# Kernel tuning notes

Measured on AMD Instinct MI355X. Metric: run time of the kernel, lower is better.

Reference implementation:

```python
import jax, jax.numpy as jnp
import numpy as np

DIM = 1024
CTX_DIM = 1024
HEADS = 16
DIM_HEAD = 64
INNER = HEADS * DIM_HEAD
SCALE = DIM_HEAD ** -0.5


def _layer_norm(x, g, b, eps=1e-5):
    mu = x.mean(-1, keepdims=True)
    var = ((x - mu) ** 2).mean(-1, keepdims=True)
    return (x - mu) * jax.lax.rsqrt(var + eps) * g + b


def setup_inputs() -> dict:
    key = jax.random.key(0)
    ks = jax.random.split(key, 10)
    b, i, j = 2, 1024, 1024
    s = lambda fan_in: 1.0 / np.sqrt(fan_in)
    return {
        "x": jax.random.normal(ks[0], (b, i, DIM), jnp.float32),
        "context": jax.random.normal(ks[1], (b, j, CTX_DIM), jnp.float32),
        "mask": jnp.ones((b, i), dtype=bool),
        "context_mask": jnp.ones((b, j), dtype=bool),
        "ln_g": jnp.ones((DIM,), jnp.float32),
        "ln_b": jnp.zeros((DIM,), jnp.float32),
        "cln_g": jnp.ones((CTX_DIM,), jnp.float32),
        "cln_b": jnp.zeros((CTX_DIM,), jnp.float32),
        "W_qk": jax.random.normal(ks[2], (DIM, INNER), jnp.float32) * s(DIM),
        "W_cqk": jax.random.normal(ks[3], (CTX_DIM, INNER), jnp.float32) * s(CTX_DIM),
        "W_v": jax.random.normal(ks[4], (DIM, INNER), jnp.float32) * s(DIM),
        "W_cv": jax.random.normal(ks[5], (CTX_DIM, INNER), jnp.float32) * s(CTX_DIM),
        "W_out": jax.random.normal(ks[6], (INNER, DIM), jnp.float32) * s(INNER),
        "b_out": jnp.zeros((DIM,), jnp.float32),
        "W_cout": jax.random.normal(ks[7], (INNER, CTX_DIM), jnp.float32) * s(INNER),
        "b_cout": jnp.zeros((CTX_DIM,), jnp.float32),
        "W_th": jax.random.normal(ks[8], (HEADS, HEADS), jnp.float32) * s(HEADS),   # talking heads [out_h, in_h]
        "W_cth": jax.random.normal(ks[9], (HEADS, HEADS), jnp.float32) * s(HEADS),
    }


def reference(x, context, mask, context_mask, ln_g, ln_b, cln_g, cln_b,
              W_qk, W_cqk, W_v, W_cv, W_out, b_out, W_cout, b_cout, W_th, W_cth):
    b, i, _ = x.shape
    j = context.shape[1]
    xn = _layer_norm(x, ln_g, ln_b)
    cn = _layer_norm(context, cln_g, cln_b)

    split = lambda t: t.reshape(t.shape[0], t.shape[1], HEADS, DIM_HEAD).transpose(0, 2, 1, 3)  # b h n d
    qk = split(xn @ W_qk)
    cqk = split(cn @ W_cqk)
    v = split(xn @ W_v)
    cv = split(cn @ W_cv)

    sim = jnp.einsum('bhid,bhjd->bhij', qk, cqk) * SCALE

    attn_mask = mask[:, None, :, None] & context_mask[:, None, None, :]  # b 1 i j
    sim = jnp.where(attn_mask, sim, -jnp.finfo(sim.dtype).max)

    attn = jax.nn.softmax(sim, axis=-1)       # rows: x attends to context
    cattn = jax.nn.softmax(sim, axis=-2)      # cols: context attends to x

    # talking heads: 1x1 conv over head dim, weight [out_h, in_h]
    attn = jnp.einsum('bhij,gh->bgij', attn, W_th)
    cattn = jnp.einsum('bhij,gh->bgij', cattn, W_cth)

    out = jnp.einsum('bhij,bhjd->bhid', attn, cv)
    cout = jnp.einsum('bhji,bhjd->bhid', cattn, v)

    merge = lambda t: t.transpose(0, 2, 1, 3).reshape(t.shape[0], t.shape[2], INNER)
    out = merge(out) @ W_out + b_out
    cout = merge(cout) @ W_cout + b_cout
    return out, cout
```

## Files before the change

kernel.cpp:

```cpp
#include <hip/hip_runtime.h>
#include <hip/hip_bf16.h>

#define BB 2
#define SEQ 1024
#define DIMD 1024
#define NH 16
#define DH 64
#define INNERD 1024
#define SCALEF 0.125f

typedef __hip_bfloat16 bf16;
typedef __attribute__((ext_vector_type(8))) short short8;
typedef __attribute__((ext_vector_type(4))) float f32x4;

__device__ __forceinline__ float b2f(bf16 x) { return __bfloat162float(x); }
__device__ __forceinline__ bf16 f2b(float x) { return __float2bfloat16(x); }
__device__ __forceinline__ float s2f(unsigned short s) {
    return __uint_as_float(((unsigned int)s) << 16);
}
__device__ __forceinline__ unsigned short f2bs(float v) {
    bf16 t = __float2bfloat16(v);
    return *(unsigned short*)&t;
}

__device__ __forceinline__ void stf(float* p, size_t i, float v) { p[i] = v; }
__device__ __forceinline__ void stf(bf16* p, size_t i, float v) { p[i] = f2b(v); }

__device__ __forceinline__ void async16(const short* g, short* l) {
    __builtin_amdgcn_global_load_lds(
        (const __attribute__((address_space(1))) unsigned int*)(g),
        (__attribute__((address_space(3))) unsigned int*)(l), 16, 0, 0);
}

__global__ __launch_bounds__(256) void prep_kernel(
    const float* __restrict__ s0, const float* __restrict__ s1,
    const float* __restrict__ s2, const float* __restrict__ s3,
    const float* __restrict__ s4, const float* __restrict__ s5,
    bf16* __restrict__ d0, bf16* __restrict__ d1, bf16* __restrict__ d2,
    bf16* __restrict__ d3, bf16* __restrict__ d4, bf16* __restrict__ d5,
    const float* __restrict__ x0, const float* __restrict__ g0,
    const float* __restrict__ b0, bf16* __restrict__ o0,
    const float* __restrict__ x1, const float* __restrict__ g1,
    const float* __restrict__ b1, bf16* __restrict__ o1) {
    int z = blockIdx.z;
    int tid = threadIdx.x;
    if (z < 6) {
        const float* W = z == 0 ? s0 : z == 1 ? s1 : z == 2 ? s2 : z == 3 ? s3
                         : z == 4 ? s4 : s5;
        bf16* Wt = z == 0 ? d0 : z == 1 ? d1 : z == 2 ? d2 : z == 3 ? d3
                   : z == 4 ? d4 : d5;
        __shared__ float T[32][33];
        int n0 = blockIdx.x * 32, k0 = blockIdx.y * 32;
        int tx = tid & 31, ty = tid >> 5;
#pragma unroll
        for (int s = 0; s < 4; ++s)
            T[ty + s * 8][tx] = W[(size_t)(k0 + ty + s * 8) * 1024 + n0 + tx];
        __syncthreads();
#pragma unroll
        for (int s = 0; s < 4; ++s)
            Wt[(size_t)(n0 + ty + s * 8) * 1024 + k0 + tx] = f2b(T[tx][ty + s * 8]);
    } else {
        int rowg = (z - 6) * 1024 + blockIdx.y * 32 + blockIdx.x;
        int sel = rowg >= BB * SEQ;
        int row = sel ? rowg - BB * SEQ : rowg;
        const float* xr = (sel ? x1 : x0) + (size_t)row * DIMD;
        const float* g = sel ? g1 : g0;
        const float* b = sel ? b1 : b0;
        bf16* orow = (sel ? o1 : o0) + (size_t)row * DIMD;
        float v[4];
        float s = 0.f, s2 = 0.f;
#pragma unroll
        for (int k = 0; k < 4; ++k) {
            v[k] = xr[tid + k * 256];
            s += v[k];
            s2 += v[k] * v[k];
        }
        __shared__ float sh1[256], sh2[256];
        sh1[tid] = s; sh2[tid] = s2;
        __syncthreads();
        for (int off = 128; off > 0; off >>= 1) {
            if (tid < off) { sh1[tid] += sh1[tid + off]; sh2[tid] += sh2[tid + off]; }
            __syncthreads();
        }
        float mu = sh1[0] * (1.f / DIMD);
        float var = sh2[0] * (1.f / DIMD) - mu * mu;
        float rstd = rsqrtf(var + 1e-5f);
#pragma unroll
        for (int k = 0; k < 4; ++k) {
            int c = tid + k * 256;
            orow[c] = f2b((v[k] - mu) * rstd * g[c] + b[c]);
        }
    }
}

template <typename TC, bool HASBIAS, int BM, int BN, int MT, int NT, int ZS, bool TRANSC>
__global__ __launch_bounds__(256) void mfma_gemm(
    const bf16* __restrict__ A, long sA1, long sA2, int lda,
    const bf16* __restrict__ Bt, long sB1, long sB2, int ldb,
    TC* __restrict__ C, long sC1, long sC2, int ldc,
    bf16* __restrict__ TD, long sT1,
    const float* __restrict__ bias0, const float* __restrict__ bias1,
    float alpha, int K) {
    constexpr int WX = BN / (NT * 16);
    static_assert((4 / WX) * MT * 16 == BM, "BM/waves mismatch");
    static_assert(BM % 64 == 0 && BN % 64 == 0, "chunk uniformity");
    int z = blockIdx.z;
    int zb = z / ZS, zh = z % ZS;
    const short* Ag = (const short*)(A + zb * sA1 + zh * sA2);
    const short* Bg = (const short*)(Bt + zb * sB1 + zh * sB2);
    TC* Cp = C + zb * sC1 + zh * sC2;
    const float* bias = (zh == 0) ? bias0 : bias1;

    const int m0 = blockIdx.y * BM;
    const int n0 = blockIdx.x * BN;
    int tid = threadIdx.x;
    int wave = tid >> 6, lane = tid & 63;
    int wm = (wave / WX) * (MT * 16), wn = (wave % WX) * (NT * 16);
    int lrow = lane & 15, lquad = lane >> 4;

    __shared__ short S[2][(BM + BN) * 32];

    f32x4 acc[MT][NT] = {};

    for (int k0 = 0; k0 < K; k0 += 64) {
        constexpr int CH = (BM + BN) / 64;
#pragma unroll
        for (int half = 0; half < 2; ++half) {
            int kh = k0 + half * 32;
#pragma unroll
            for (int ch = 0; ch < CH; ++ch) {
                int e = ch * 256 + tid;
                int r = e >> 2, c = (e & 3) * 8;
                const short* g = (r < BM)
                                     ? Ag + (size_t)(m0 + r) * lda + kh + c
                                     : Bg + (size_t)(n0 + r - BM) * ldb + kh + c;
                async16(g, S[half] + (size_t)e * 8);
            }
        }
        __syncthreads();
#pragma unroll
        for (int half = 0; half < 2; ++half) {
            short8 af[MT], bfv[NT];
#pragma unroll
            for (int mt = 0; mt < MT; ++mt)
                af[mt] = *(const short8*)(S[half] + (wm + mt * 16 + lrow) * 32 +
                                          lquad * 8);
#pragma unroll
            for (int nt = 0; nt < NT; ++nt)
                bfv[nt] = *(const short8*)(S[half] + (BM + wn + nt * 16 + lrow) * 32 +
                                           lquad * 8);
#pragma unroll
            for (int mt = 0; mt < MT; ++mt)
#pragma unroll
                for (int nt = 0; nt < NT; ++nt)
                    acc[mt][nt] = __builtin_amdgcn_mfma_f32_16x16x32_bf16(
                        af[mt], bfv[nt], acc[mt][nt], 0, 0, 0);
        }
        __syncthreads();
    }
    if (TRANSC && zh == 1) {
        bf16* td = TD + zb * sT1;
        int bsel = m0 >> 10;
        int tokb = (m0 & 1023) + wm + lquad * 4;
#pragma unroll
        for (int mt = 0; mt < MT; ++mt) {
#pragma unroll
            for (int nt = 0; nt < NT; ++nt) {
                int col = n0 + wn + nt * 16 + lrow;
                ushort4 o;
                o.x = f2bs(acc[mt][nt][0]);
                o.y = f2bs(acc[mt][nt][1]);
                o.z = f2bs(acc[mt][nt][2]);
                o.w = f2bs(acc[mt][nt][3]);
                *(ushort4*)((unsigned short*)td +
                            ((size_t)(bsel * NH + (col >> 6)) * DH + (col & 63)) * SEQ +
                            tokb + mt * 16) = o;
            }
        }
        return;
    }
#pragma unroll
    for (int mt = 0; mt < MT; ++mt) {
#pragma unroll
        for (int nt = 0; nt < NT; ++nt) {
            int col = n0 + wn + nt * 16 + lrow;
#pragma unroll
            for (int r = 0; r < 4; ++r) {
                int row = m0 + wm + mt * 16 + lquad * 4 + r;
                float v = acc[mt][nt][r] * alpha;
                if (HASBIAS) v += bias[col];
                stf(Cp, (size_t)row * ldc + col, v);
            }
        }
    }
}

__global__ __launch_bounds__(256) void qkt_stats_kernel(
    const bf16* __restrict__ qk, const bf16* __restrict__ cqk,
    bf16* __restrict__ sim16, float* __restrict__ rowPart,
    float* __restrict__ colPart, long sQ, long sS, long sP) {
    int z = blockIdx.z;
    int b = z >> 4, h = z & 15;
    const short* Ag = (const short*)(qk + b * sQ + h * DH);
    const short* Bg = (const short*)(cqk + b * sQ + h * DH);
    bf16* Cp = sim16 + b * sS + (size_t)h * SEQ * SEQ;
    rowPart += b * sP;
    colPart += b * sP;

    const int m0 = blockIdx.y * 128;
    const int n0 = blockIdx.x * 128;
    int tid = threadIdx.x;
    int wave = tid >> 6, lane = tid & 63;
    int wy = wave >> 1, wx = wave & 1;
    int wm = wy * 64, wn = wx * 64;
    int lrow = lane & 15, lquad = lane >> 4;

    __shared__ short S[2][256 * 32];
    __shared__ float rowLDS[128][2];
    __shared__ float colLDS[128][2];

    f32x4 acc[4][4] = {};

#pragma unroll
    for (int half = 0; half < 2; ++half) {
        int kh = half * 32;
#pragma unroll
        for (int ch = 0; ch < 4; ++ch) {
            int e = ch * 256 + tid;
            int r = e >> 2, c = (e & 3) * 8;
            const short* g = (r < 128)
                                 ? Ag + (size_t)(m0 + r) * INNERD + kh + c
                                 : Bg + (size_t)(n0 + r - 128) * INNERD + kh + c;
            async16(g, S[half] + (size_t)e * 8);
        }
    }
    __syncthreads();
#pragma unroll
    for (int half = 0; half < 2; ++half) {
        short8 af[4], bfv[4];
#pragma unroll
        for (int mt = 0; mt < 4; ++mt)
            af[mt] = *(const short8*)(S[half] + (wm + mt * 16 + lrow) * 32 + lquad * 8);
#pragma unroll
        for (int nt = 0; nt < 4; ++nt)
            bfv[nt] = *(const short8*)(S[half] + (128 + wn + nt * 16 + lrow) * 32 +
                                       lquad * 8);
#pragma unroll
        for (int mt = 0; mt < 4; ++mt)
#pragma unroll
            for (int nt = 0; nt < 4; ++nt)
                acc[mt][nt] = __builtin_amdgcn_mfma_f32_16x16x32_bf16(
                    af[mt], bfv[nt], acc[mt][nt], 0, 0, 0);
    }
    float rband[16];
    float cacc[4] = {};
#pragma unroll
    for (int k = 0; k < 16; ++k) rband[k] = 0.f;
#pragma unroll
    for (int mt = 0; mt < 4; ++mt) {
#pragma unroll
        for (int nt = 0; nt < 4; ++nt) {
            int col = n0 + wn + nt * 16 + lrow;
#pragma unroll
            for (int r = 0; r < 4; ++r) {
                int row = m0 + wm + mt * 16 + lquad * 4 + r;
                unsigned short us = f2bs(acc[mt][nt][r] * SCALEF);
                *((unsigned short*)Cp + (size_t)row * SEQ + col) = us;
                float e = __expf(s2f(us));
                rband[mt * 4 + r] += e;
                cacc[nt] += e;
            }
        }
    }
#pragma unroll
    for (int m = 1; m < 16; m <<= 1)
#pragma unroll
        for (int k = 0; k < 16; ++k) rband[k] += __shfl_xor(rband[k], m, 64);
    if (lrow == 0) {
#pragma unroll
        for (int mt = 0; mt < 4; ++mt)
#pragma unroll
            for (int r = 0; r < 4; ++r)
                rowLDS[wm + mt * 16 + lquad * 4 + r][wx] = rband[mt * 4 + r];
    }
#pragma unroll
    for (int m = 16; m < 64; m <<= 1)
#pragma unroll
        for (int nt = 0; nt < 4; ++nt) cacc[nt] += __shfl_xor(cacc[nt], m, 64);
    if (lquad == 0) {
#pragma unroll
        for (int nt = 0; nt < 4; ++nt)
            colLDS[wn + nt * 16 + lrow][wy] = cacc[nt];
    }
    __syncthreads();
    if (tid < 128)
        rowPart[((size_t)h * 8 + blockIdx.x) * SEQ + m0 + tid] =
            rowLDS[tid][0] + rowLDS[tid][1];
    else
        colPart[((size_t)h * 8 + blockIdx.y) * SEQ + n0 + tid - 128] =
            colLDS[tid - 128][0] + colLDS[tid - 128][1];
}

__global__ __launch_bounds__(256) void finish_inv2_kernel(const float* __restrict__ partA,
                                                          float* __restrict__ invA,
                                                          const float* __restrict__ partB,
                                                          float* __restrict__ invB) {
    int idx = blockIdx.x * 256 + threadIdx.x;
    int h = idx >> 10, t = idx & 1023;
    float sA = 0.f, sB = 0.f;
#pragma unroll
    for (int p = 0; p < 8; ++p) {
        sA += partA[((size_t)h * 8 + p) * SEQ + t];
        sB += partB[((size_t)h * 8 + p) * SEQ + t];
    }
    invA[idx] = 1.f / sA;
    invB[idx] = 1.f / sB;
}

__global__ __launch_bounds__(256) void mix_kernel(bf16* simattn,
                                                  bf16* __restrict__ catT,
                                                  const float* __restrict__ rli,
                                                  const float* __restrict__ cli,
                                                  const float* __restrict__ Wth,
                                                  const float* __restrict__ Wcth,
                                                  long sS, long sI) {
    int zb = blockIdx.z;
    simattn += zb * sS;
    catT += zb * sS;
    rli += zb * sI;
    cli += zb * sI;
    int d = blockIdx.y * gridDim.x + blockIdx.x;
    int grp = d >> 4, s = d & 15;
    int pairIdx = grp * 8 + (s & 7);
    int half = s >> 3;
    int j0 = (2 * (pairIdx & 31) + half) * 16;
    int i0 = (pairIdx >> 5) * 16;
    int tid = threadIdx.x;
    int jl = tid & 15, il = tid >> 4;
    int i = i0 + il, j = j0 + jl;
    float sa[16] = {}, sc[16] = {};
#pragma unroll
    for (int h = 0; h < 16; ++h) {
        float s2 = b2f(simattn[((size_t)h * SEQ + i) * SEQ + j]);
        float e = __expf(s2);
        float p = e * rli[h * SEQ + i];
        float q = e * cli[h * SEQ + j];
#pragma unroll
        for (int g = 0; g < 16; ++g) {
            sa[g] += p * Wth[g * 16 + h];
            sc[g] += q * Wcth[g * 16 + h];
        }
    }
#pragma unroll
    for (int g = 0; g < 16; ++g)
        simattn[((size_t)g * SEQ + i) * SEQ + j] = f2b(sa[g]);
    __shared__ float T[16][16][17];
#pragma unroll
    for (int g = 0; g < 16; ++g) T[g][il][jl] = sc[g];
    __syncthreads();
#pragma unroll
    for (int g = 0; g < 16; ++g)
        catT[((size_t)g * SEQ + j0 + il) * SEQ + i0 + jl] = f2b(T[g][jl][il]);
}

extern "C" void kernel_launch(void* const* d_in, const int* in_sizes, int n_in,
                              void* d_out, int out_size, void* d_ws, size_t ws_size,
                              hipStream_t stream) {
    const float* x = (const float*)d_in[0];
    const float* ctx = (const float*)d_in[1];
    const float* ln_g = (const float*)d_in[4];
    const float* ln_b = (const float*)d_in[5];
    const float* cln_g = (const float*)d_in[6];
    const float* cln_b = (const float*)d_in[7];
    const float* W_qk = (const float*)d_in[8];
    const float* W_cqk = (const float*)d_in[9];
    const float* W_v = (const float*)d_in[10];
    const float* W_cv = (const float*)d_in[11];
    const float* W_out = (const float*)d_in[12];
    const float* b_out = (const float*)d_in[13];
    const float* W_cout = (const float*)d_in[14];
    const float* b_cout = (const float*)d_in[15];
    const float* W_th = (const float*)d_in[16];
    const float* W_cth = (const float*)d_in[17];
    float* out = (float*)d_out;

    char* ws = (char*)d_ws;
    size_t off = 0;
    auto alloc = [&](size_t bytes) {
        void* p = ws + off;
        off += (bytes + 255) & ~(size_t)255;
        return p;
    };
    const size_t NTOK = (size_t)BB * SEQ * DIMD;
    const size_t WSZ = (size_t)DIMD * INNERD;
    const size_t U = (size_t)NH * SEQ * SEQ;
    const long HB = (long)NH * DH * SEQ;

    bf16* xn = (bf16*)alloc(NTOK * 2);
    bf16* cn = (bf16*)alloc(NTOK * 2);
    bf16* qk = (bf16*)alloc(NTOK * 2);
    bf16* cqk = (bf16*)alloc(NTOK * 2);
    bf16* wqk_t = (bf16*)alloc(WSZ * 2);
    bf16* wv_t = (bf16*)alloc(WSZ * 2);
    bf16* wcqk_t = (bf16*)alloc(WSZ * 2);
    bf16* wcv_t = (bf16*)alloc(WSZ * 2);
    bf16* wout_t = (bf16*)alloc(WSZ * 2);
    bf16* wcout_t = (bf16*)alloc(WSZ * 2);
    bf16* cvT = (bf16*)alloc(NTOK * 2);
    bf16* vT = (bf16*)alloc(NTOK * 2);
    bf16* outm = xn;

    const size_t partB = (size_t)NH * 8 * SEQ * 4;
    const size_t invB = (size_t)NH * SEQ * 4;
    const size_t bigNeed = 4 * U * 2 + 2 * (2 * partB) + 2 * (2 * invB);
    bool big = (ws_size > off) && (ws_size - off >= bigNeed);

    prep_kernel<<<dim3(32, 32, 10), 256, 0, stream>>>(
        W_qk, W_v, W_cqk, W_cv, W_out, W_cout,
        wqk_t, wv_t, wcqk_t, wcv_t, wout_t, wcout_t,
        x, ln_g, ln_b, xn, ctx, cln_g, cln_b, cn);
    mfma_gemm<bf16, false, 128, 64, 2, 4, 2, true><<<dim3(16, 16, 4), 256, 0, stream>>>(
        xn, (long)NTOK, 0, DIMD,
        wqk_t, (long)(2 * WSZ), (long)WSZ, DIMD,
        qk, (long)NTOK, 0, INNERD,
        vT, -(long)NTOK,
        nullptr, nullptr, 1.0f, DIMD);

    if (big) {
        bf16* sim0 = (bf16*)alloc(U * 2);
        bf16* sim1 = (bf16*)alloc(U * 2);
        bf16* cb0 = (bf16*)alloc(U * 2);
        bf16* cb1 = (bf16*)alloc(U * 2);
        float* rowPart = (float*)alloc(2 * partB);
        float* colPart = (float*)alloc(2 * partB);
        float* rowInv = (float*)alloc(2 * invB);
        float* colInv = (float*)alloc(2 * invB);
        (void)sim1; (void)cb1;

        qkt_stats_kernel<<<dim3(8, 8, 32), 256, 0, stream>>>(
            qk, cqk, sim0, rowPart, colPart,
            (long)SEQ * INNERD, (long)U, (long)NH * 8 * SEQ);
        finish_inv2_kernel<<<2 * NH * SEQ / 256, 256, 0, stream>>>(rowPart, rowInv,
                                                                   colPart, colInv);
        mix_kernel<<<dim3(SEQ / 16, SEQ / 16, 2), 256, 0, stream>>>(
            sim0, cb0, rowInv, colInv, W_th, W_cth, (long)U, (long)NH * SEQ);
        mfma_gemm<bf16, false, 64, 64, 1, 4, 16, false><<<dim3(1, 16, 4 * NH), 256, 0,
                                                          stream>>>(
            sim0, (long)U, (long)SEQ * SEQ, SEQ,
            cvT, HB, (long)DH * SEQ, SEQ,
            outm, (long)SEQ * INNERD, (long)DH, INNERD,
            nullptr, 0, nullptr, nullptr, 1.0f, SEQ);
    } else {
        bf16* simA = (bf16*)alloc(U * 2);
        bf16* cbuf = (bf16*)alloc(U * 2);
        float* rowPart = (float*)alloc(partB);
        float* colPart = (float*)alloc(partB);
        float* rowInv = (float*)alloc(invB);
        float* colInv = (float*)alloc(invB);
        for (int b = 0; b < BB; ++b) {
            qkt_stats_kernel<<<dim3(8, 8, 16), 256, 0, stream>>>(
                qk + (size_t)b * SEQ * INNERD, cqk + (size_t)b * SEQ * INNERD,
                simA, rowPart, colPart, 0, 0, 0);
            finish_inv2_kernel<<<NH * SEQ / 256, 256, 0, stream>>>(rowPart, rowInv,
                                                                   colPart, colInv);
            mix_kernel<<<dim3(SEQ / 16, SEQ / 16, 1), 256, 0, stream>>>(
                simA, cbuf, rowInv, colInv, W_th, W_cth, 0, 0);
            mfma_gemm<bf16, false, 64, 64, 1, 4, 16, false><<<dim3(1, 16, 2 * NH), 256,
                                                              0, stream>>>(
                simA, (long)U, (long)SEQ * SEQ, SEQ,
                cvT + (size_t)b * HB, (long)NTOK, (long)DH * SEQ, SEQ,
                outm + (size_t)b * SEQ * INNERD, (long)NTOK, (long)DH, INNERD,
                nullptr, 0, nullptr, nullptr, 1.0f, SEQ);
        }
    }

    mfma_gemm<float, true, 128, 64, 2, 4, 2, false><<<dim3(16, 16, 2), 256, 0, stream>>>(
        outm, 0, (long)NTOK, INNERD, wout_t, 0, (long)WSZ, INNERD,
        out, 0, (long)NTOK, DIMD, nullptr, 0, b_out, b_cout, 1.0f, INNERD);
}
```

Before: 279.1 us.

## Compute talking-heads head mixing with MFMA bf16 instead of scalar FMAs

The per-element 16x16 head-mixing loop in the softmax/talking-heads kernel is replaced by two 16x16x32 bf16 MFMA instructions per row, with half the K dimension zero-padded. Each wave handles four i-rows, and lanes in the upper half of the wave feed zeros. The transposed cattn output is now staged through shared memory and written as 16-byte vector stores. The exp/normalize products and the weights are rounded to bf16 before mixing, which adds precision loss, and half of each MFMA's K lanes do no useful work.

```diff
diff --git a/kernel.cpp b/kernel.cpp
--- a/kernel.cpp
+++ b/kernel.cpp
@@ -336,31 +336,63 @@
     int j0 = (2 * (pairIdx & 31) + half) * 16;
     int i0 = (pairIdx >> 5) * 16;
     int tid = threadIdx.x;
-    int jl = tid & 15, il = tid >> 4;
-    int i = i0 + il, j = j0 + jl;
-    float sa[16] = {}, sc[16] = {};
-#pragma unroll
-    for (int h = 0; h < 16; ++h) {
-        float s2 = b2f(simattn[((size_t)h * SEQ + i) * SEQ + j]);
-        float e = __expf(s2);
-        float p = e * rli[h * SEQ + i];
-        float q = e * cli[h * SEQ + j];
-#pragma unroll
-        for (int g = 0; g < 16; ++g) {
-            sa[g] += p * Wth[g * 16 + h];
-            sc[g] += q * Wcth[g * 16 + h];
-        }
-    }
-#pragma unroll
-    for (int g = 0; g < 16; ++g)
-        simattn[((size_t)g * SEQ + i) * SEQ + j] = f2b(sa[g]);
-    __shared__ float T[16][16][17];
-#pragma unroll
-    for (int g = 0; g < 16; ++g) T[g][il][jl] = sc[g];
+    int wave = tid >> 6, lane = tid & 63;
+    int q = lane >> 4, low = lane & 15;
+    int j = j0 + low;
+
+    short8 aTH = {}, aCTH = {};
+    float clv[8];
+    if (q < 2) {
+#pragma unroll
+        for (int idx = 0; idx < 8; ++idx) {
+            int h = q * 8 + idx;
+            aTH[idx] = (short)f2bs(Wth[low * 16 + h]);
+            aCTH[idx] = (short)f2bs(Wcth[low * 16 + h]);
+            clv[idx] = cli[h * SEQ + j];
+        }
+    }
+
+    __shared__ float Tc[16][16][17];
+
+    const unsigned short* sp = (const unsigned short*)simattn;
+    unsigned short* ap = (unsigned short*)simattn;
+
+#pragma unroll
+    for (int rr = 0; rr < 4; ++rr) {
+        int il = wave * 4 + rr;
+        int i = i0 + il;
+        short8 bp = {}, bq = {};
+        if (q < 2) {
+            const unsigned short* sr =
+                sp + (size_t)(q * 8) * SEQ * SEQ + (size_t)i * SEQ + j;
+            const float* rp = rli + (size_t)(q * 8) * SEQ + i;
+#pragma unroll
+            for (int idx = 0; idx < 8; ++idx) {
+                float e = __expf(s2f(sr[(size_t)idx * SEQ * SEQ]));
+                bp[idx] = (short)f2bs(e * rp[(size_t)idx * SEQ]);
+                bq[idx] = (short)f2bs(e * clv[idx]);
+            }
+        }
+        f32x4 z = {};
+        f32x4 accA = __builtin_amdgcn_mfma_f32_16x16x32_bf16(aTH, bp, z, 0, 0, 0);
+        f32x4 accC = __builtin_amdgcn_mfma_f32_16x16x32_bf16(aCTH, bq, z, 0, 0, 0);
+#pragma unroll
+        for (int r = 0; r < 4; ++r) {
+            ap[((size_t)(q * 4 + r) * SEQ + i) * SEQ + j] = f2bs(accA[r]);
+            Tc[il][q * 4 + r][low] = accC[r];
+        }
+    }
     __syncthreads();
-#pragma unroll
-    for (int g = 0; g < 16; ++g)
-        catT[((size_t)g * SEQ + j0 + il) * SEQ + i0 + jl] = f2b(T[g][jl][il]);
+    int gp = tid >> 4, jp = tid & 15;
+    short8 o0, o1;
+#pragma unroll
+    for (int k = 0; k < 8; ++k) o0[k] = (short)f2bs(Tc[k][gp][jp]);
+#pragma unroll
+    for (int k = 0; k < 8; ++k) o1[k] = (short)f2bs(Tc[k + 8][gp][jp]);
+    unsigned short* dst =
+        (unsigned short*)catT + ((size_t)gp * SEQ + j0 + jp) * SEQ + i0;
+    *(short8*)dst = o0;
+    *(short8*)(dst + 8) = o1;
 }
 
 extern "C" void kernel_launch(void* const* d_in, const int* in_sizes, int n_in,
```

Measured after the change: 294.3 us. +5.5%, slower.

## Fuse softmax exp, talking-heads mix and PV GEMM into one split-K kernel

Applied to the files above, without the earlier changes.

Replaces the separate mix kernel (which wrote the mixed row-attention and a transposed column-attention matrix back to global memory) and the following PV GEMM with a single fused kernel. It recomputes exp and normalization from the stored logits, applies the head-mixing weights with MFMA into shared memory, and immediately multiplies by the value tiles. Each block covers a slice of K, so partial results are combined with fp32 atomics into a zeroed buffer, and a cast kernel then converts that buffer to bf16. This removes two full-size attention-matrix round trips to memory, at the cost of a memset, atomic contention and an extra cast pass; it also drops the small-workspace fallback path.

```diff
diff --git a/kernel.cpp b/kernel.cpp
--- a/kernel.cpp
+++ b/kernel.cpp
@@ -317,50 +317,151 @@
     invB[idx] = 1.f / sB;
 }
 
-__global__ __launch_bounds__(256) void mix_kernel(bf16* simattn,
-                                                  bf16* __restrict__ catT,
-                                                  const float* __restrict__ rli,
-                                                  const float* __restrict__ cli,
-                                                  const float* __restrict__ Wth,
-                                                  const float* __restrict__ Wcth,
-                                                  long sS, long sI) {
-    int zb = blockIdx.z;
-    simattn += zb * sS;
-    catT += zb * sS;
-    rli += zb * sI;
-    cli += zb * sI;
-    int d = blockIdx.y * gridDim.x + blockIdx.x;
-    int grp = d >> 4, s = d & 15;
-    int pairIdx = grp * 8 + (s & 7);
-    int half = s >> 3;
-    int j0 = (2 * (pairIdx & 31) + half) * 16;
-    int i0 = (pairIdx >> 5) * 16;
-    int tid = threadIdx.x;
-    int jl = tid & 15, il = tid >> 4;
-    int i = i0 + il, j = j0 + jl;
-    float sa[16] = {}, sc[16] = {};
-#pragma unroll
-    for (int h = 0; h < 16; ++h) {
-        float s2 = b2f(simattn[((size_t)h * SEQ + i) * SEQ + j]);
-        float e = __expf(s2);
-        float p = e * rli[h * SEQ + i];
-        float q = e * cli[h * SEQ + j];
-#pragma unroll
-        for (int g = 0; g < 16; ++g) {
-            sa[g] += p * Wth[g * 16 + h];
-            sc[g] += q * Wcth[g * 16 + h];
-        }
-    }
-#pragma unroll
-    for (int g = 0; g < 16; ++g)
-        simattn[((size_t)g * SEQ + i) * SEQ + j] = f2b(sa[g]);
-    __shared__ float T[16][16][17];
-#pragma unroll
-    for (int g = 0; g < 16; ++g) T[g][il][jl] = sc[g];
-    __syncthreads();
-#pragma unroll
-    for (int g = 0; g < 16; ++g)
-        catT[((size_t)g * SEQ + j0 + il) * SEQ + i0 + jl] = f2b(T[g][jl][il]);
+__global__ __launch_bounds__(256) void fused_pv(
+    const bf16* __restrict__ sim, const float* __restrict__ rowInv,
+    const float* __restrict__ colInv, const float* __restrict__ Wth,
+    const float* __restrict__ Wcth, const bf16* __restrict__ cvT,
+    float* __restrict__ outF) {
+    const int z = blockIdx.z;
+    const int path = z >> 1, b = z & 1;
+    const unsigned short* sp =
+        (const unsigned short*)sim + (size_t)b * NH * SEQ * SEQ;
+    const float* inv = (path ? colInv : rowInv) + (size_t)b * NH * SEQ;
+    const float* Wmix = path ? Wcth : Wth;
+    const short* Bg = (const short*)cvT + (size_t)z * NH * DH * SEQ;
+    outF += (size_t)z * SEQ * INNERD;
+
+    const int bx = blockIdx.x;
+    const int rt = (bx & 7) * 8 + (bx >> 3);
+    const int r0 = rt * 16;
+    const int kbase = blockIdx.y * 256;
+
+    const int tid = threadIdx.x;
+    const int wave = tid >> 6, lane = tid & 63;
+    const int q = lane >> 4, low = lane & 15;
+    const bool loQ = q < 2;
+    const int hq = (q & 1) * 8;
+
+    constexpr int HsA = 584, IsA = 36;
+    constexpr int HsC = 644, KsC = 20;
+    constexpr int Gs = 656, Rs = 40;
+    __shared__ unsigned short RAW[10304];
+    __shared__ unsigned short ATT[10496];
+
+    float s8[8];
+    {
+        const float* ip = inv + (size_t)hq * SEQ + r0 + low;
+#pragma unroll
+        for (int idx = 0; idx < 8; ++idx) s8[idx] = ip[(size_t)idx * SEQ];
+    }
+    short8 aW = {};
+    if (loQ) {
+#pragma unroll
+        for (int idx = 0; idx < 8; ++idx)
+            aW[idx] = (short)f2bs(Wmix[low * 16 + hq + idx]);
+    }
+
+    f32x4 acc[4][4] = {};
+    const int gw = wave * 4;
+
+    for (int st = 0; st < 8; ++st) {
+        const int k0 = kbase + st * 32;
+        if (path == 0) {
+#pragma unroll
+            for (int it = 0; it < 4; ++it) {
+                int rowId = it * 64 + (tid >> 2);
+                int h = rowId >> 4, r = rowId & 15, p = tid & 3;
+                const unsigned short* src =
+                    sp + ((size_t)h * SEQ + r0 + r) * SEQ + k0 + p * 8;
+                int4 w = *(const int4*)src;
+                unsigned short* d = RAW + h * HsA + r * IsA + p * 8;
+                *(int2*)d = make_int2(w.x, w.y);
+                *(int2*)(d + 4) = make_int2(w.z, w.w);
+            }
+        } else {
+#pragma unroll
+            for (int it = 0; it < 4; ++it) {
+                int task = it * 256 + tid;
+                int row = task >> 1, p = task & 1;
+                int h = row >> 5, kk = row & 31;
+                const unsigned short* src =
+                    sp + ((size_t)h * SEQ + k0 + kk) * SEQ + r0 + p * 8;
+                int4 w = *(const int4*)src;
+                unsigned short* d = RAW + h * HsC + kk * KsC + p * 8;
+                *(int2*)d = make_int2(w.x, w.y);
+                *(int2*)(d + 4) = make_int2(w.z, w.w);
+            }
+        }
+        __syncthreads();
+#pragma unroll
+        for (int u = 0; u < 4; ++u) {
+            int kq = wave * 8 + 2 * u + (q >> 1);
+            short8 P;
+#pragma unroll
+            for (int idx = 0; idx < 8; ++idx) {
+                unsigned short uu =
+                    (path == 0) ? RAW[(hq + idx) * HsA + low * IsA + kq]
+                                : RAW[(hq + idx) * HsC + kq * KsC + low];
+                float e = __expf(s2f(uu));
+                P[idx] = (short)f2bs(e * s8[idx]);
+            }
+            int4 Pi = *(int4*)&P;
+            int4 Sw;
+            Sw.x = __shfl_xor(Pi.x, 32);
+            Sw.y = __shfl_xor(Pi.y, 32);
+            Sw.z = __shfl_xor(Pi.z, 32);
+            Sw.w = __shfl_xor(Pi.w, 32);
+            short8 z8 = {};
+            short8 bpE = loQ ? P : z8;
+            short8 bpO = loQ ? *(short8*)&Sw : z8;
+            f32x4 zz = {};
+            f32x4 dE = __builtin_amdgcn_mfma_f32_16x16x32_bf16(aW, bpE, zz, 0, 0, 0);
+            f32x4 dO = __builtin_amdgcn_mfma_f32_16x16x32_bf16(aW, bpO, zz, 0, 0, 0);
+            int kE = wave * 8 + 2 * u;
+#pragma unroll
+            for (int rr = 0; rr < 4; ++rr) {
+                ATT[(q * 4 + rr) * Gs + low * Rs + kE] = f2bs(dE[rr]);
+                ATT[(q * 4 + rr) * Gs + low * Rs + kE + 1] = f2bs(dO[rr]);
+            }
+        }
+        __syncthreads();
+#pragma unroll
+        for (int gg = 0; gg < 4; ++gg) {
+            int g = gw + gg;
+            short8 af = *(const short8*)(ATT + g * Gs + low * Rs + q * 8);
+#pragma unroll
+            for (int dt = 0; dt < 4; ++dt) {
+                const short* bp =
+                    Bg + ((size_t)(g * 64 + dt * 16 + low)) * SEQ + k0 + q * 8;
+                short8 bf8 = *(const short8*)bp;
+                acc[gg][dt] = __builtin_amdgcn_mfma_f32_16x16x32_bf16(
+                    af, bf8, acc[gg][dt], 0, 0, 0);
+            }
+        }
+        __syncthreads();
+    }
+#pragma unroll
+    for (int gg = 0; gg < 4; ++gg)
+#pragma unroll
+        for (int dt = 0; dt < 4; ++dt)
+#pragma unroll
+            for (int rr = 0; rr < 4; ++rr)
+                unsafeAtomicAdd(outF + (size_t)(r0 + q * 4 + rr) * INNERD +
+                                    (gw + gg) * 64 + dt * 16 + low,
+                                acc[gg][dt][rr]);
+}
+
+__global__ __launch_bounds__(256) void cast_kernel(const float* __restrict__ src,
+                                                   bf16* __restrict__ dst) {
+    size_t i = ((size_t)blockIdx.x * 256 + threadIdx.x) * 8;
+    float4 a = *(const float4*)(src + i);
+    float4 c = *(const float4*)(src + i + 4);
+    short8 o;
+    o[0] = (short)f2bs(a.x); o[1] = (short)f2bs(a.y);
+    o[2] = (short)f2bs(a.z); o[3] = (short)f2bs(a.w);
+    o[4] = (short)f2bs(c.x); o[5] = (short)f2bs(c.y);
+    o[6] = (short)f2bs(c.z); o[7] = (short)f2bs(c.w);
+    *(short8*)((unsigned short*)dst + i) = o;
 }
 
 extern "C" void kernel_launch(void* const* d_in, const int* in_sizes, int n_in,
@@ -409,11 +510,21 @@
     bf16* cvT = (bf16*)alloc(NTOK * 2);
     bf16* vT = (bf16*)alloc(NTOK * 2);
     bf16* outm = xn;
+    (void)cn; (void)vT;
 
     const size_t partB = (size_t)NH * 8 * SEQ * 4;
     const size_t invB = (size_t)NH * SEQ * 4;
-    const size_t bigNeed = 4 * U * 2 + 2 * (2 * partB) + 2 * (2 * invB);
-    bool big = (ws_size > off) && (ws_size - off >= bigNeed);
+
+    bf16* sim0 = (bf16*)alloc(U * 2);
+    bf16* sim1 = (bf16*)alloc(U * 2);
+    (void)sim1;
+    float* rowPart = (float*)alloc(2 * partB);
+    float* colPart = (float*)alloc(2 * partB);
+    float* rowInv = (float*)alloc(2 * invB);
+    float* colInv = (float*)alloc(2 * invB);
+    float* outF = (float*)alloc((size_t)4 * SEQ * INNERD * 4);
+
+    hipMemsetAsync(outF, 0, (size_t)4 * SEQ * INNERD * 4, stream);
 
     prep_kernel<<<dim3(32, 32, 10), 256, 0, stream>>>(
         W_qk, W_v, W_cqk, W_cv, W_out, W_cout,
@@ -426,53 +537,16 @@
         vT, -(long)NTOK,
         nullptr, nullptr, 1.0f, DIMD);
 
-    if (big) {
-        bf16* sim0 = (bf16*)alloc(U * 2);
-        bf16* sim1 = (bf16*)alloc(U * 2);
-        bf16* cb0 = (bf16*)alloc(U * 2);
-        bf16* cb1 = (bf16*)alloc(U * 2);
-        float* rowPart = (float*)alloc(2 * partB);
-        float* colPart = (float*)alloc(2 * partB);
-        float* rowInv = (float*)alloc(2 * invB);
-        float* colInv = (float*)alloc(2 * invB);
-        (void)sim1; (void)cb1;
-
-        qkt_stats_kernel<<<dim3(8, 8, 32), 256, 0, stream>>>(
-            qk, cqk, sim0, rowPart, colPart,
-            (long)SEQ * INNERD, (long)U, (long)NH * 8 * SEQ);
-        finish_inv2_kernel<<<2 * NH * SEQ / 256, 256, 0, stream>>>(rowPart, rowInv,
-                                                                   colPart, colInv);
-        mix_kernel<<<dim3(SEQ / 16, SEQ / 16, 2), 256, 0, stream>>>(
-            sim0, cb0, rowInv, colInv, W_th, W_cth, (long)U, (long)NH * SEQ);
-        mfma_gemm<bf16, false, 64, 64, 1, 4, 16, false><<<dim3(1, 16, 4 * NH), 256, 0,
-                                                          stream>>>(
-            sim0, (long)U, (long)SEQ * SEQ, SEQ,
-            cvT, HB, (long)DH * SEQ, SEQ,
-            outm, (long)SEQ * INNERD, (long)DH, INNERD,
-            nullptr, 0, nullptr, nullptr, 1.0f, SEQ);
-    } else {
-        bf16* simA = (bf16*)alloc(U * 2);
-        bf16* cbuf = (bf16*)alloc(U * 2);
-        float* rowPart = (float*)alloc(partB);
-        float* colPart = (float*)alloc(partB);
-        float* rowInv = (float*)alloc(invB);
-        float* colInv = (float*)alloc(invB);
-        for (int b = 0; b < BB; ++b) {
-            qkt_stats_kernel<<<dim3(8, 8, 16), 256, 0, stream>>>(
-                qk + (size_t)b * SEQ * INNERD, cqk + (size_t)b * SEQ * INNERD,
-                simA, rowPart, colPart, 0, 0, 0);
-            finish_inv2_kernel<<<NH * SEQ / 256, 256, 0, stream>>>(rowPart, rowInv,
-                                                                   colPart, colInv);
-            mix_kernel<<<dim3(SEQ / 16, SEQ / 16, 1), 256, 0, stream>>>(
-                simA, cbuf, rowInv, colInv, W_th, W_cth, 0, 0);
-            mfma_gemm<bf16, false, 64, 64, 1, 4, 16, false><<<dim3(1, 16, 2 * NH), 256,
-                                                              0, stream>>>(
-                simA, (long)U, (long)SEQ * SEQ, SEQ,
-                cvT + (size_t)b * HB, (long)NTOK, (long)DH * SEQ, SEQ,
-                outm + (size_t)b * SEQ * INNERD, (long)NTOK, (long)DH, INNERD,
-                nullptr, 0, nullptr, nullptr, 1.0f, SEQ);
-        }
-    }
+    qkt_stats_kernel<<<dim3(8, 8, 32), 256, 0, stream>>>(
+        qk, cqk, sim0, rowPart, colPart,
+        (long)SEQ * INNERD, (long)U, (long)NH * 8 * SEQ);
+    finish_inv2_kernel<<<2 * NH * SEQ / 256, 256, 0, stream>>>(rowPart, rowInv,
+                                                               colPart, colInv);
+    fused_pv<<<dim3(64, 4, 4), 256, 0, stream>>>(
+        sim0, rowInv, colInv, W_th, W_cth, cvT, outF);
+
+    cast_kernel<<<(int)((size_t)4 * SEQ * INNERD / (256 * 8)), 256, 0, stream>>>(
+        outF, outm);
 
     mfma_gemm<float, true, 128, 64, 2, 4, 2, false><<<dim3(16, 16, 2), 256, 0, stream>>>(
         outm, 0, (long)NTOK, INNERD, wout_t, 0, (long)WSZ, INNERD,
```

New measurement: 321.5 us. 15.2% more time.

## Widen mix kernel tiles to 16x32 with packed bf16x2 loads and stores

Applied to the files above, without the earlier changes.

The talking-heads mix kernel now has each thread handle two adjacent columns, using 32-bit packed bf16 loads and stores. It stages the row and column softmax inverses in shared memory. The transposed cattn output is written through a two-pass shared-memory transpose with 16-byte vector stores. The intent is to cut memory transactions and global loads in this bandwidth-bound kernel, in exchange for doubled register accumulators and extra barriers.

```diff
diff --git a/kernel.cpp b/kernel.cpp
--- a/kernel.cpp
+++ b/kernel.cpp
@@ -333,34 +333,72 @@
     int grp = d >> 4, s = d & 15;
     int pairIdx = grp * 8 + (s & 7);
     int half = s >> 3;
-    int j0 = (2 * (pairIdx & 31) + half) * 16;
-    int i0 = (pairIdx >> 5) * 16;
+    int j0 = (pairIdx & 31) * 32;
+    int i0 = (((pairIdx >> 5) << 1) + half) * 16;
     int tid = threadIdx.x;
-    int jl = tid & 15, il = tid >> 4;
-    int i = i0 + il, j = j0 + jl;
-    float sa[16] = {}, sc[16] = {};
+    int il = tid >> 4, jp = tid & 15;
+
+    __shared__ float Tc[8][16][33];
+    __shared__ float rli_l[16][16];
+    __shared__ float cli_l[16][32];
+
+    rli_l[tid >> 4][tid & 15] = rli[(size_t)(tid >> 4) * SEQ + i0 + (tid & 15)];
+#pragma unroll
+    for (int k = 0; k < 2; ++k) {
+        int c = k * 256 + tid;
+        cli_l[c >> 5][c & 31] = cli[(size_t)(c >> 5) * SEQ + j0 + (c & 31)];
+    }
+    __syncthreads();
+
+    const unsigned int* lp = (const unsigned int*)simattn +
+                             (((size_t)(i0 + il) * SEQ + j0) >> 1) + jp;
+    float sa0[16] = {}, sa1[16] = {}, sc0[16] = {}, sc1[16] = {};
 #pragma unroll
     for (int h = 0; h < 16; ++h) {
-        float s2 = b2f(simattn[((size_t)h * SEQ + i) * SEQ + j]);
-        float e = __expf(s2);
-        float p = e * rli[h * SEQ + i];
-        float q = e * cli[h * SEQ + j];
+        unsigned int v = lp[(size_t)h * (SEQ * SEQ / 2)];
+        float e0 = __expf(s2f((unsigned short)(v & 0xffffu)));
+        float e1 = __expf(s2f((unsigned short)(v >> 16)));
+        float r = rli_l[h][il];
+        float p0 = e0 * r, p1 = e1 * r;
+        float q0 = e0 * cli_l[h][2 * jp], q1 = e1 * cli_l[h][2 * jp + 1];
 #pragma unroll
         for (int g = 0; g < 16; ++g) {
-            sa[g] += p * Wth[g * 16 + h];
-            sc[g] += q * Wcth[g * 16 + h];
-        }
-    }
+            float w = Wth[g * 16 + h];
+            float wc = Wcth[g * 16 + h];
+            sa0[g] += p0 * w;
+            sa1[g] += p1 * w;
+            sc0[g] += q0 * wc;
+            sc1[g] += q1 * wc;
+        }
+    }
+    unsigned int* ap = (unsigned int*)simattn;
+    size_t aoff = (((size_t)(i0 + il) * SEQ + j0) >> 1) + jp;
 #pragma unroll
     for (int g = 0; g < 16; ++g)
-        simattn[((size_t)g * SEQ + i) * SEQ + j] = f2b(sa[g]);
-    __shared__ float T[16][16][17];
-#pragma unroll
-    for (int g = 0; g < 16; ++g) T[g][il][jl] = sc[g];
-    __syncthreads();
-#pragma unroll
-    for (int g = 0; g < 16; ++g)
-        catT[((size_t)g * SEQ + j0 + il) * SEQ + i0 + jl] = f2b(T[g][jl][il]);
+        ap[(size_t)g * (SEQ * SEQ / 2) + aoff] =
+            (unsigned int)f2bs(sa0[g]) | ((unsigned int)f2bs(sa1[g]) << 16);
+
+    unsigned int* cp = (unsigned int*)catT;
+    int gl = tid >> 5, jl = tid & 31;
+#pragma unroll
+    for (int ch = 0; ch < 2; ++ch) {
+        __syncthreads();
+#pragma unroll
+        for (int g = 0; g < 8; ++g) {
+            Tc[g][il][2 * jp] = (ch ? sc0[8 + g] : sc0[g]);
+            Tc[g][il][2 * jp + 1] = (ch ? sc1[8 + g] : sc1[g]);
+        }
+        __syncthreads();
+        int g = ch * 8 + gl;
+        unsigned int o[8];
+#pragma unroll
+        for (int ip = 0; ip < 8; ++ip)
+            o[ip] = (unsigned int)f2bs(Tc[gl][2 * ip][jl]) |
+                    ((unsigned int)f2bs(Tc[gl][2 * ip + 1][jl]) << 16);
+        size_t cb = (size_t)g * (SEQ * SEQ / 2) + (((size_t)(j0 + jl) * SEQ + i0) >> 1);
+        *(uint4*)(cp + cb) = make_uint4(o[0], o[1], o[2], o[3]);
+        *(uint4*)(cp + cb + 4) = make_uint4(o[4], o[5], o[6], o[7]);
+    }
 }
 
 extern "C" void kernel_launch(void* const* d_in, const int* in_sizes, int n_in,
@@ -442,7 +480,7 @@
             (long)SEQ * INNERD, (long)U, (long)NH * 8 * SEQ);
         finish_inv2_kernel<<<2 * NH * SEQ / 256, 256, 0, stream>>>(rowPart, rowInv,
                                                                    colPart, colInv);
-        mix_kernel<<<dim3(SEQ / 16, SEQ / 16, 2), 256, 0, stream>>>(
+        mix_kernel<<<dim3(32, 64, 2), 256, 0, stream>>>(
             sim0, cb0, rowInv, colInv, W_th, W_cth, (long)U, (long)NH * SEQ);
         mfma_gemm<bf16, false, 64, 64, 1, 4, 16, false><<<dim3(1, 16, 4 * NH), 256, 0,
                                                           stream>>>(
@@ -463,7 +501,7 @@
                 simA, rowPart, colPart, 0, 0, 0);
             finish_inv2_kernel<<<NH * SEQ / 256, 256, 0, stream>>>(rowPart, rowInv,
                                                                    colPart, colInv);
-            mix_kernel<<<dim3(SEQ / 16, SEQ / 16, 1), 256, 0, stream>>>(
+            mix_kernel<<<dim3(32, 64, 1), 256, 0, stream>>>(
                 simA, cbuf, rowInv, colInv, W_th, W_cth, 0, 0);
             mfma_gemm<bf16, false, 64, 64, 1, 4, 16, false><<<dim3(1, 16, 2 * NH), 256,
                                                               0, stream>>>(
```

Result: no change. 278.8 us (-0.1%).
